# Optimization experiments

Measured on AMD Instinct MI355X. Metric: run time of the kernel, lower is better.

The kernel has to match this reference:

```python
import jax, jax.numpy as jnp
import numpy as np

EPS = 1e-6
NH, DK, DV = 4, 32, 32

def _ln2d(x, w, b):
    # LayerNorm2d: normalize over channel dim (dim=1), biased variance
    mu = jnp.mean(x, axis=1, keepdims=True)
    var = jnp.mean((x - mu) ** 2, axis=1, keepdims=True)
    y = (x - mu) / jnp.sqrt(var + EPS)
    return w[None, :, None, None] * y + b[None, :, None, None]

def _c1x1(w, x):
    # 1x1 conv == per-pixel matmul: w [out,in], x [B,C,H,W]
    return jnp.einsum('oc,bchw->bohw', w, x)

def _shifts(x, r):
    # All (2r+1)^2 zero-padded spatial shifts, row-major (dy,dx) like nn.Unfold.
    B, C, H, W = x.shape
    xp = jnp.pad(x, ((0, 0), (0, 0), (r, r), (r, r)))
    return jnp.stack([xp[:, :, dy:dy + H, dx:dx + W]
                      for dy in range(2 * r + 1) for dx in range(2 * r + 1)], axis=0)

def _local_attn(q, k, v, kernel):
    # Correlation-pyramid local attention: per-pixel q.k over kxk window of k,
    # softmax over window (temperature sqrt(d_k)), weighted sum of v window
    # (weights shared across channels, per ChannelAttention).
    B, _, H, W = q.shape
    r = (kernel - 1) // 2
    K2 = kernel * kernel
    qh = q.reshape(B, NH, DK, H, W)
    ks = _shifts(k, r).reshape(K2, B, NH, DK, H, W)
    corr = jnp.einsum('bncyx,jbncyx->jbnyx', qh, ks)            # [K2,B,NH,H,W]
    attn = jax.nn.softmax(corr / jnp.sqrt(jnp.float32(DK)), axis=0)
    vs = _shifts(v, r).reshape(K2, B, NH, DV, H, W)
    out = jnp.einsum('jbnyx,jbncyx->bncyx', attn, vs)
    return out.reshape(B, NH * DV, H, W)

def _mha(q, k, v, kernel, wq, wk, wv, fc, lnw, lnb):
    resid = q
    heads = _local_attn(_c1x1(wq, q), _c1x1(wk, k), _c1x1(wv, v), kernel)
    out = _c1x1(fc, heads) + resid   # residual BEFORE LN (per source)
    return _ln2d(out, lnw, lnb)

def _ffn(x, w1, b1, w2, b2, lnw, lnb):
    h = jax.nn.relu(_c1x1(w1, x) + b1[None, :, None, None])
    y = _c1x1(w2, h) + b2[None, :, None, None]
    return _ln2d(y, lnw, lnb) + x    # LN BEFORE residual add (per source)

def setup_inputs():
    key = jax.random.key(0)
    ks = jax.random.split(key, 24)
    B, C, H, W = 4, 128, 96, 96
    s = (2.0 / C) ** 0.5
    f = jnp.float32
    return {
        'input1': jax.random.normal(ks[0], (B, C, H, W), f),
        'input2': jax.random.normal(ks[1], (B, C, H, W), f),
        'wq_s': jax.random.normal(ks[2], (NH * DK, C), f) * s,
        'wk_s': jax.random.normal(ks[3], (NH * DK, C), f) * s,
        'wv_s': jax.random.normal(ks[4], (NH * DV, C), f) * s,
        'fc_s': jax.random.normal(ks[5], (C, NH * DV), f) * s,
        'lnw_s': jnp.ones((C,), f),
        'lnb_s': jnp.zeros((C,), f),
        'wq_c': jax.random.normal(ks[6], (NH * DK, C), f) * s,
        'wk_c': jax.random.normal(ks[7], (NH * DK, C), f) * s,
        'wv_c': jax.random.normal(ks[8], (NH * DV, C), f) * s,
        'fc_c': jax.random.normal(ks[9], (C, NH * DV), f) * s,
        'lnw_c': jnp.ones((C,), f),
        'lnb_c': jnp.zeros((C,), f),
        'w1': jax.random.normal(ks[10], (C, C), f) * s,
        'b1': jnp.zeros((C,), f),
        'w2': jax.random.normal(ks[11], (C, C), f) * s,
        'b2': jnp.zeros((C,), f),
        'lnw_f': jnp.ones((C,), f),
        'lnb_f': jnp.zeros((C,), f),
        'kernel': 5,
        'pad': 2,
    }

def reference(input1, input2, wq_s, wk_s, wv_s, fc_s, lnw_s, lnb_s,
              wq_c, wk_c, wv_c, fc_c, lnw_c, lnb_c,
              w1, b1, w2, b2, lnw_f, lnb_f, kernel, pad):
    slf1 = _mha(input1, input1, input1, kernel, wq_s, wk_s, wv_s, fc_s, lnw_s, lnb_s)
    slf2 = _mha(input2, input2, input2, kernel, wq_s, wk_s, wv_s, fc_s, lnw_s, lnb_s)
    crs1 = _mha(slf1, slf2, slf2, kernel, wq_c, wk_c, wv_c, fc_c, lnw_c, lnb_c)
    crs2 = _mha(slf2, slf1, slf1, kernel, wq_c, wk_c, wv_c, fc_c, lnw_c, lnb_c)
    out1 = _ffn(crs1, w1, b1, w2, b2, lnw_f, lnb_f)
    out2 = _ffn(crs2, w1, b1, w2, b2, lnw_f, lnb_f)
    return (out1, out2)
```

## Files before the change

### kernel.cpp

```cpp
#include <hip/hip_runtime.h>
#include <hip/hip_bf16.h>

typedef _Float16 h16;
typedef __attribute__((ext_vector_type(8))) _Float16 f16x8v;
typedef __attribute__((ext_vector_type(2))) _Float16 h2v;
typedef __attribute__((ext_vector_type(4))) float f32x4;
#define DI __device__ __forceinline__

constexpr int CH = 128;
constexpr int HH = 96, WW = 96;
constexpr int HW = HH * WW;
constexpr int NB = 4;
constexpr int NPIX = NB * HW;
constexpr int LDT = 136;
constexpr size_t HP = (size_t)NPIX * 32;
constexpr int GH = NPIX / 64;
constexpr int TY = 4, TX = 32;
constexpr int HYH = TY + 4, HXH = TX + 4;
constexpr int LDC = 40;
constexpr int ATB = NPIX / (TY * TX) * 4;

struct __attribute__((aligned(16))) h16x8 { h16 h[8]; };
struct Set { h16 *q, *k, *v; };

DI float h2f(h16 x) { return (float)x; }
DI h16   f2h(float x) { return (h16)x; }


DI void stage_x_pl(const float* __restrict__ src, h16* xl, int t) {
    #pragma unroll
    for (int i = 0; i < 8; ++i) {
        int id = t + 256 * i, c = id >> 4, p4 = (id & 15) * 4;
        float4 v = *reinterpret_cast<const float4*>(&src[(size_t)c * HW + p4]);
        xl[(p4 + 0) * LDT + c] = f2h(v.x);
        xl[(p4 + 1) * LDT + c] = f2h(v.y);
        xl[(p4 + 2) * LDT + c] = f2h(v.z);
        xl[(p4 + 3) * LDT + c] = f2h(v.w);
    }
}

DI void stage_x_hm(const h16* __restrict__ Tq, h16* xl, int p0, int t) {
    const int px = t >> 2, c8 = (t & 3) * 8;
    #pragma unroll
    for (int h = 0; h < 4; ++h)
        *reinterpret_cast<f16x8v*>(&xl[px * LDT + h * 32 + c8]) =
            *reinterpret_cast<const f16x8v*>(&Tq[(size_t)h * HP + (size_t)(p0 + px) * 32 + c8]);
}

DI void stage_w(const float* __restrict__ w, h16* wl, int t) {
    #pragma unroll
    for (int i = 0; i < 8; ++i) {
        int id = t + 256 * i, o = id >> 4, cc = (id & 15) * 8;
        float4 a = *reinterpret_cast<const float4*>(&w[o * CH + cc]);
        float4 b = *reinterpret_cast<const float4*>(&w[o * CH + cc + 4]);
        h16x8 tmp;
        tmp.h[0] = f2h(a.x); tmp.h[1] = f2h(a.y); tmp.h[2] = f2h(a.z); tmp.h[3] = f2h(a.w);
        tmp.h[4] = f2h(b.x); tmp.h[5] = f2h(b.y); tmp.h[6] = f2h(b.z); tmp.h[7] = f2h(b.w);
        *reinterpret_cast<f16x8v*>(&wl[o * LDT + cc]) = *reinterpret_cast<const f16x8v*>(&tmp);
    }
}

DI void wload(const float* __restrict__ w, f16x8v* pre, int t) {
    #pragma unroll
    for (int i = 0; i < 8; ++i) {
        int id = t + 256 * i, o = id >> 4, cc = (id & 15) * 8;
        float4 a = *reinterpret_cast<const float4*>(&w[o * CH + cc]);
        float4 b = *reinterpret_cast<const float4*>(&w[o * CH + cc + 4]);
        h16x8 tmp;
        tmp.h[0] = f2h(a.x); tmp.h[1] = f2h(a.y); tmp.h[2] = f2h(a.z); tmp.h[3] = f2h(a.w);
        tmp.h[4] = f2h(b.x); tmp.h[5] = f2h(b.y); tmp.h[6] = f2h(b.z); tmp.h[7] = f2h(b.w);
        pre[i] = *reinterpret_cast<const f16x8v*>(&tmp);
    }
}
DI void wcommit(const f16x8v* pre, h16* wl, int t) {
    #pragma unroll
    for (int i = 0; i < 8; ++i) {
        int id = t + 256 * i, o = id >> 4, cc = (id & 15) * 8;
        *reinterpret_cast<f16x8v*>(&wl[o * LDT + cc]) = pre[i];
    }
}

DI void rload(const float* __restrict__ src, float4* rpre, int t) {
    #pragma unroll
    for (int i = 0; i < 8; ++i) {
        int id = t + 256 * i, c = id >> 4, p4 = (id & 15) * 4;
        rpre[i] = *reinterpret_cast<const float4*>(&src[(size_t)c * HW + p4]);
    }
}
DI void rcommit(const float4* rpre, float* rl, int t) {
    #pragma unroll
    for (int i = 0; i < 8; ++i) {
        int id = t + 256 * i, c = id >> 4, p4 = (id & 15) * 4;
        rl[c * 65 + p4 + 0] = rpre[i].x;
        rl[c * 65 + p4 + 1] = rpre[i].y;
        rl[c * 65 + p4 + 2] = rpre[i].z;
        rl[c * 65 + p4 + 3] = rpre[i].w;
    }
}

DI void gemm64(const h16* xl, const h16* wl, int w, int l, f32x4* acc) {
    const int s = l & 15, g = l >> 4;
    #pragma unroll
    for (int ks = 0; ks < 4; ++ks) {
        f16x8v a = *reinterpret_cast<const f16x8v*>(&xl[(16 * w + s) * LDT + ks * 32 + g * 8]);
        #pragma unroll
        for (int n = 0; n < 8; ++n) {
            f16x8v b = *reinterpret_cast<const f16x8v*>(&wl[(16 * n + s) * LDT + ks * 32 + g * 8]);
            acc[n] = __builtin_amdgcn_mfma_f32_16x16x32_f16(a, b, acc[n], 0, 0, 0);
        }
    }
}

DI void qkv_epi(const f32x4* acc, h16* comp, int p0, int w, int l) {
    const int s = l & 15, g = l >> 4;
    #pragma unroll
    for (int n = 0; n < 8; ++n) {
        const int o = 16 * n + s, head = o >> 5, ch = o & 31;
        h16* pl = comp + (size_t)head * HP;
        #pragma unroll
        for (int j = 0; j < 4; ++j) {
            int px = 16 * w + 4 * g + j;
            pl[(size_t)(p0 + px) * 32 + ch] = f2h(acc[n][j]);
        }
    }
}

DI void ln128(float r[8][4], const float* gm, const float* bt, float val[8][4]) {
    #pragma unroll
    for (int j = 0; j < 4; ++j) {
        float sm = 0.f, sq = 0.f;
        #pragma unroll
        for (int n = 0; n < 8; ++n) { float v = r[n][j]; sm += v; sq += v * v; }
        sm += __shfl_xor(sm, 1); sq += __shfl_xor(sq, 1);
        sm += __shfl_xor(sm, 2); sq += __shfl_xor(sq, 2);
        sm += __shfl_xor(sm, 4); sq += __shfl_xor(sq, 4);
        sm += __shfl_xor(sm, 8); sq += __shfl_xor(sq, 8);
        const float mu = sm * (1.f / 128.f);
        const float var = sq * (1.f / 128.f) - mu * mu;
        const float rs = rsqrtf(var + 1e-6f);
        #pragma unroll
        for (int n = 0; n < 8; ++n)
            val[n][j] = gm[n] * (r[n][j] - mu) * rs + bt[n];
    }
}

__global__ __launch_bounds__(256, 2)
void qkv_self_b(const float* __restrict__ x0, const float* __restrict__ x1,
                const float* __restrict__ w0, const float* __restrict__ w1_,
                const float* __restrict__ w2_, Set sA, Set sB) {
    __shared__ h16 xl[64 * LDT];
    __shared__ h16 wl[CH * LDT];
    const int bid = blockIdx.x, half = bid / GH, p0 = (bid % GH) * 64;
    const float* xv = half ? x1 : x0;
    Set S = half ? sB : sA;
    const int t = threadIdx.x;
    const int b = p0 / HW, hw0 = p0 % HW;
    stage_x_pl(xv + (size_t)b * CH * HW + hw0, xl, t);
    stage_w(w0, wl, t);
    __syncthreads();
    const int w = t >> 6, l = t & 63;

    f16x8v pre[8];
    #pragma unroll
    for (int m = 0; m < 3; ++m) {
        h16* comp = (m == 0) ? S.q : ((m == 1) ? S.k : S.v);
        if (m == 0) wload(w1_, pre, t);
        if (m == 1) wload(w2_, pre, t);
        f32x4 acc[8];
        #pragma unroll
        for (int n = 0; n < 8; ++n) acc[n] = {0.f, 0.f, 0.f, 0.f};
        gemm64(xl, wl, w, l, acc);
        qkv_epi(acc, comp, p0, w, l);
        if (m < 2) {
            __syncthreads();
            wcommit(pre, wl, t);
            __syncthreads();
        }
    }
}

__global__ __launch_bounds__(256)
void attn5b(Set s0, Set s1) {
    __shared__ h16 kv[HYH * HXH * LDC];
    const int bid = blockIdx.x, setId = bid / ATB, id = bid - setId * ATB;
    Set S = setId ? s1 : s0;
    const int n = id & 3, tile = id >> 2;
    const int img = tile / 72, rem = tile % 72, tr = rem / 3, tc = rem % 3;
    const int y0 = tr * TY, x0 = tc * TX;
    const int t = threadIdx.x;
    const int p = t >> 1, half = t & 1, ch16 = half * 16;
    const int ty = p >> 5, tx = p & 31;
    h16* Qh = S.q + (size_t)n * HP;
    const h16* Kh = S.k + (size_t)n * HP;
    const h16* Vh = S.v + (size_t)n * HP;
    const int gp = img * HW + (y0 + ty) * WW + (x0 + tx);
    h16* qp = Qh + (size_t)gp * 32 + ch16;

    f16x8v q0 = *reinterpret_cast<const f16x8v*>(qp);
    f16x8v q1 = *reinterpret_cast<const f16x8v*>(qp + 8);
    {
        const h16 sc = (h16)0.17677669529663689f;
        #pragma unroll
        for (int e = 0; e < 8; ++e) { q0[e] *= sc; q1[e] *= sc; }
    }

    #pragma unroll
    for (int i = 0; i < 5; ++i) {
        int id2 = t + 256 * i;
        if (id2 < 1152) {
            int r = id2 / 144, c = id2 - r * 144, px = c >> 2, c8 = (c & 3) * 8;
            int y = y0 + r - 2, x = x0 + px - 2;
            f16x8v v = {0, 0, 0, 0, 0, 0, 0, 0};
            if ((unsigned)y < (unsigned)HH && (unsigned)x < (unsigned)WW)
                v = *reinterpret_cast<const f16x8v*>(&Kh[((size_t)(img * HW + y * WW + x)) * 32 + c8]);
            *reinterpret_cast<f16x8v*>(&kv[(r * HXH + px) * LDC + c8]) = v;
        }
    }
    __syncthreads();

    float corr[25];
    #pragma unroll
    for (int dy = 0; dy < 5; ++dy)
        #pragma unroll
        for (int dx = 0; dx < 5; ++dx) {
            const h16* kp = &kv[((ty + dy) * HXH + tx + dx) * LDC + ch16];
            f16x8v k0 = *reinterpret_cast<const f16x8v*>(kp);
            f16x8v k1 = *reinterpret_cast<const f16x8v*>(kp + 8);
            float s;
#if __has_builtin(__builtin_amdgcn_fdot2)
            s = __builtin_amdgcn_fdot2(h2v{q0[0], q0[1]}, h2v{k0[0], k0[1]}, 0.f, false);
            s = __builtin_amdgcn_fdot2(h2v{q0[2], q0[3]}, h2v{k0[2], k0[3]}, s, false);
            s = __builtin_amdgcn_fdot2(h2v{q0[4], q0[5]}, h2v{k0[4], k0[5]}, s, false);
            s = __builtin_amdgcn_fdot2(h2v{q0[6], q0[7]}, h2v{k0[6], k0[7]}, s, false);
            s = __builtin_amdgcn_fdot2(h2v{q1[0], q1[1]}, h2v{k1[0], k1[1]}, s, false);
            s = __builtin_amdgcn_fdot2(h2v{q1[2], q1[3]}, h2v{k1[2], k1[3]}, s, false);
            s = __builtin_amdgcn_fdot2(h2v{q1[4], q1[5]}, h2v{k1[4], k1[5]}, s, false);
            s = __builtin_amdgcn_fdot2(h2v{q1[6], q1[7]}, h2v{k1[6], k1[7]}, s, false);
#else
            s = 0.f;
            #pragma unroll
            for (int e = 0; e < 8; ++e) s += h2f(q0[e]) * h2f(k0[e]);
            #pragma unroll
            for (int e = 0; e < 8; ++e) s += h2f(q1[e]) * h2f(k1[e]);
#endif
            s += __shfl_xor(s, 1);
            corr[dy * 5 + dx] = s;
        }

    float m = corr[0];
    #pragma unroll
    for (int j = 1; j < 25; ++j) m = fmaxf(m, corr[j]);
    float sum = 0.f;
    #pragma unroll
    for (int j = 0; j < 25; ++j) {
        float e = __expf(corr[j] - m);
        corr[j] = e; sum += e;
    }
    const float inv = 1.f / sum;

    __syncthreads();
    #pragma unroll
    for (int i = 0; i < 5; ++i) {
        int id2 = t + 256 * i;
        if (id2 < 1152) {
            int r = id2 / 144, c = id2 - r * 144, px = c >> 2, c8 = (c & 3) * 8;
            int y = y0 + r - 2, x = x0 + px - 2;
            f16x8v v = {0, 0, 0, 0, 0, 0, 0, 0};
            if ((unsigned)y < (unsigned)HH && (unsigned)x < (unsigned)WW)
                v = *reinterpret_cast<const f16x8v*>(&Vh[((size_t)(img * HW + y * WW + x)) * 32 + c8]);
            *reinterpret_cast<f16x8v*>(&kv[(r * HXH + px) * LDC + c8]) = v;
        }
    }
    __syncthreads();

    f16x8v o0 = {0, 0, 0, 0, 0, 0, 0, 0};
    f16x8v o1 = {0, 0, 0, 0, 0, 0, 0, 0};
    #pragma unroll
    for (int dy = 0; dy < 5; ++dy)
        #pragma unroll
        for (int dx = 0; dx < 5; ++dx) {
            const h16 ah = f2h(corr[dy * 5 + dx]);
            const f16x8v av = {ah, ah, ah, ah, ah, ah, ah, ah};
            const h16* vp = &kv[((ty + dy) * HXH + tx + dx) * LDC + ch16];
            f16x8v v0 = *reinterpret_cast<const f16x8v*>(vp);
            f16x8v v1 = *reinterpret_cast<const f16x8v*>(vp + 8);
            o0 += av * v0;
            o1 += av * v1;
        }
    {
        const h16 ih = f2h(inv);
        const f16x8v iv = {ih, ih, ih, ih, ih, ih, ih, ih};
        o0 *= iv; o1 *= iv;
    }
    *reinterpret_cast<f16x8v*>(qp)     = o0;
    *reinterpret_cast<f16x8v*>(qp + 8) = o1;
}

__global__ __launch_bounds__(256, 2)
void fcx1_b(const h16* __restrict__ tA, const h16* __restrict__ tB,
            const float* __restrict__ in1, const float* __restrict__ in2,
            const float* __restrict__ wfc, const float* __restrict__ gamma,
            const float* __restrict__ beta,
            const float* __restrict__ wq, const float* __restrict__ wk,
            const float* __restrict__ wv,
            h16* __restrict__ x1g, h16* __restrict__ x2g, Set c1, Set c2) {
    __shared__ h16 xl[64 * LDT];
    __shared__ __align__(16) char wsm[CH * LDT * 2];
    h16*   wl = (h16*)wsm;
    float* rl = (float*)wsm;
    const int bid = blockIdx.x, half = bid / GH, p0 = (bid % GH) * 64;
    const h16*   tin = half ? tB : tA;
    const float* inr = half ? in2 : in1;
    h16*         xg  = half ? x2g : x1g;
    Set own   = half ? c2 : c1;
    Set other = half ? c1 : c2;
    const int t = threadIdx.x;
    const int w = t >> 6, l = t & 63, s = l & 15, g4 = l >> 4;
    const int b = p0 / HW, hw0 = p0 % HW;

    stage_x_hm(tin, xl, p0, t);
    stage_w(wfc, wl, t);
    float4 rpre[8];
    rload(inr + (size_t)b * CH * HW + hw0, rpre, t);
    __syncthreads();

    f32x4 accF[8];
    #pragma unroll
    for (int n = 0; n < 8; ++n) accF[n] = {0.f, 0.f, 0.f, 0.f};
    gemm64(xl, wl, w, l, accF);
    __syncthreads();

    rcommit(rpre, rl, t);
    f16x8v pre[8];
    wload(wq, pre, t);
    __syncthreads();

    h16 vX[8][4];
    {
        float gm[8], bt[8], r[8][4], val[8][4];
        #pragma unroll
        for (int n = 0; n < 8; ++n) { gm[n] = gamma[16 * n + s]; bt[n] = beta[16 * n + s]; }
        #pragma unroll
        for (int n = 0; n < 8; ++n) {
            const int o = 16 * n + s;
            #pragma unroll
            for (int j = 0; j < 4; ++j) {
                const int px = 16 * w + 4 * g4 + j;
                r[n][j] = accF[n][j] + rl[o * 65 + px];
            }
        }
        ln128(r, gm, bt, val);
        #pragma unroll
        for (int n = 0; n < 8; ++n)
            #pragma unroll
            for (int j = 0; j < 4; ++j) vX[n][j] = f2h(val[n][j]);
    }
    __syncthreads();
    #pragma unroll
    for (int n = 0; n < 8; ++n) {
        const int o = 16 * n + s;
        #pragma unroll
        for (int j = 0; j < 4; ++j) {
            const int px = 16 * w + 4 * g4 + j;
            xl[px * LDT + o] = vX[n][j];
            xg[(size_t)(p0 + px) * CH + o] = vX[n][j];
        }
    }
    wcommit(pre, wl, t);
    __syncthreads();
    {
        f32x4 acc[8];
        #pragma unroll
        for (int n = 0; n < 8; ++n) acc[n] = {0.f, 0.f, 0.f, 0.f};
        wload(wk, pre, t);
        gemm64(xl, wl, w, l, acc);
        qkv_epi(acc, own.q, p0, w, l);
    }
    __syncthreads();
    wcommit(pre, wl, t);
    __syncthreads();
    {
        f32x4 acc[8];
        #pragma unroll
        for (int n = 0; n < 8; ++n) acc[n] = {0.f, 0.f, 0.f, 0.f};
        wload(wv, pre, t);
        gemm64(xl, wl, w, l, acc);
        qkv_epi(acc, other.k, p0, w, l);
    }
    __syncthreads();
    wcommit(pre, wl, t);
    __syncthreads();
    {
        f32x4 acc[8];
        #pragma unroll
        for (int n = 0; n < 8; ++n) acc[n] = {0.f, 0.f, 0.f, 0.f};
        gemm64(xl, wl, w, l, acc);
        qkv_epi(acc, other.v, p0, w, l);
    }
}

__global__ __launch_bounds__(256, 2)
void ffn_ln_b(const h16* __restrict__ t0, const h16* __restrict__ t1,
              const h16* __restrict__ x0, const h16* __restrict__ x1,
              const float* __restrict__ wfc, const float* __restrict__ gc,
              const float* __restrict__ bc,
              const float* __restrict__ w1m, const float* __restrict__ b1v,
              const float* __restrict__ w2m, const float* __restrict__ b2v,
              const float* __restrict__ gf, const float* __restrict__ bf,
              float* __restrict__ o0, float* __restrict__ o1) {
    __shared__ __align__(16) char smem[64 * LDT * 2 * 2 + CH * LDT * 2];
    h16*   xl = (h16*)smem;
    h16*   yl = (h16*)(smem + 64 * LDT * 2);
    h16*   wl = (h16*)(smem + 64 * LDT * 2 * 2);
    float* ll = (float*)(smem + 64 * LDT * 2 * 2);
    const int bid = blockIdx.x, half = bid / GH, p0 = (bid % GH) * 64;
    const h16* tin = half ? t1 : t0;
    const h16* xg  = half ? x1 : x0;
    float* outp = half ? o1 : o0;
    const int t = threadIdx.x;
    const int w = t >> 6, l = t & 63, s = l & 15, g4 = l >> 4;

    stage_x_hm(tin, xl, p0, t);
    stage_w(wfc, wl, t);
    __syncthreads();

    h16 yv[8][4];
    {
        f32x4 acc[8];
        #pragma unroll
        for (int n = 0; n < 8; ++n) acc[n] = {0.f, 0.f, 0.f, 0.f};
        gemm64(xl, wl, w, l, acc);
        float gm[8], bt[8], r[8][4], val[8][4];
        #pragma unroll
        for (int n = 0; n < 8; ++n) { gm[n] = gc[16 * n + s]; bt[n] = bc[16 * n + s]; }
        #pragma unroll
        for (int n = 0; n < 8; ++n) {
            const int o = 16 * n + s;
            #pragma unroll
            for (int j = 0; j < 4; ++j) {
                const int px = 16 * w + 4 * g4 + j;
                r[n][j] = acc[n][j] + h2f(xg[(size_t)(p0 + px) * CH + o]);
            }
        }
        ln128(r, gm, bt, val);
        #pragma unroll
        for (int n = 0; n < 8; ++n)
            #pragma unroll
            for (int j = 0; j < 4; ++j) yv[n][j] = f2h(val[n][j]);
    }
    __syncthreads();
    #pragma unroll
    for (int n = 0; n < 8; ++n) {
        const int o = 16 * n + s;
        #pragma unroll
        for (int j = 0; j < 4; ++j)
            yl[(16 * w + 4 * g4 + j) * LDT + o] = yv[n][j];
    }
    stage_w(w1m, wl, t);
    __syncthreads();

    {
        f32x4 acc[8];
        #pragma unroll
        for (int n = 0; n < 8; ++n) acc[n] = {0.f, 0.f, 0.f, 0.f};
        gemm64(yl, wl, w, l, acc);
        #pragma unroll
        for (int n = 0; n < 8; ++n) {
            const int o = 16 * n + s;
            const float bv = b1v[o];
            #pragma unroll
            for (int j = 0; j < 4; ++j)
                xl[(16 * w + 4 * g4 + j) * LDT + o] = f2h(fmaxf(acc[n][j] + bv, 0.f));
        }
    }
    __syncthreads();
    stage_w(w2m, wl, t);
    __syncthreads();

    float val[8][4];
    {
        f32x4 acc[8];
        #pragma unroll
        for (int n = 0; n < 8; ++n) acc[n] = {0.f, 0.f, 0.f, 0.f};
        gemm64(xl, wl, w, l, acc);
        float gm[8], bt[8], r[8][4];
        #pragma unroll
        for (int n = 0; n < 8; ++n) { gm[n] = gf[16 * n + s]; bt[n] = bf[16 * n + s]; }
        #pragma unroll
        for (int n = 0; n < 8; ++n) {
            const int o = 16 * n + s;
            const float bv = b2v[o];
            #pragma unroll
            for (int j = 0; j < 4; ++j) r[n][j] = acc[n][j] + bv;
        }
        ln128(r, gm, bt, val);
        #pragma unroll
        for (int n = 0; n < 8; ++n) {
            const int o = 16 * n + s;
            #pragma unroll
            for (int j = 0; j < 4; ++j)
                val[n][j] += h2f(yl[(16 * w + 4 * g4 + j) * LDT + o]);
        }
    }
    __syncthreads();
    #pragma unroll
    for (int n = 0; n < 8; ++n) {
        const int o = 16 * n + s;
        #pragma unroll
        for (int j = 0; j < 4; ++j) ll[o * 65 + 16 * w + 4 * g4 + j] = val[n][j];
    }
    __syncthreads();
    const int b = p0 / HW, hw0 = p0 % HW;
    #pragma unroll
    for (int i = 0; i < 8; ++i) {
        int id = t + 256 * i, c = id >> 4, p4 = (id & 15) * 4;
        float4 v = { ll[c * 65 + p4], ll[c * 65 + p4 + 1],
                     ll[c * 65 + p4 + 2], ll[c * 65 + p4 + 3] };
        *reinterpret_cast<float4*>(&outp[(size_t)b * CH * HW + (size_t)c * HW + hw0 + p4]) = v;
    }
}

extern "C" void kernel_launch(void* const* d_in, const int* in_sizes, int n_in,
                              void* d_out, int out_size, void* d_ws, size_t ws_size,
                              hipStream_t stream) {
    (void)in_sizes; (void)n_in; (void)out_size; (void)ws_size;
    const float* in1  = (const float*)d_in[0];
    const float* in2  = (const float*)d_in[1];
    const float* wq_s = (const float*)d_in[2];
    const float* wk_s = (const float*)d_in[3];
    const float* wv_s = (const float*)d_in[4];
    const float* fc_s = (const float*)d_in[5];
    const float* lnw_s= (const float*)d_in[6];
    const float* lnb_s= (const float*)d_in[7];
    const float* wq_c = (const float*)d_in[8];
    const float* wk_c = (const float*)d_in[9];
    const float* wv_c = (const float*)d_in[10];
    const float* fc_c = (const float*)d_in[11];
    const float* lnw_c= (const float*)d_in[12];
    const float* lnb_c= (const float*)d_in[13];
    const float* w1   = (const float*)d_in[14];
    const float* b1   = (const float*)d_in[15];
    const float* w2   = (const float*)d_in[16];
    const float* b2   = (const float*)d_in[17];
    const float* lnw_f= (const float*)d_in[18];
    const float* lnb_f= (const float*)d_in[19];

    const size_t BUF  = (size_t)NPIX * CH;
    const size_t BUFB = BUF * 2;
    char* ws = (char*)d_ws;
    h16* W0 = (h16*)(ws + 0 * BUFB);
    h16* W1 = (h16*)(ws + 1 * BUFB);
    h16* W2 = (h16*)(ws + 2 * BUFB);
    h16* W3 = (h16*)(ws + 3 * BUFB);
    h16* D0 = (h16*)d_out;
    h16* D1 = (h16*)((char*)d_out + 1 * BUFB);
    h16* D2 = (h16*)((char*)d_out + 2 * BUFB);
    h16* D3 = (h16*)((char*)d_out + 3 * BUFB);
    float* out1 = (float*)d_out;
    float* out2 = (float*)d_out + BUF;

    const dim3 B(256);

    Set SA = {W0, D0, D1};
    Set SB = {W1, D2, D3};
    h16* X1 = W2;
    h16* X2 = W3;
    Set C1 = {W0, D0, D1};
    Set C2 = {W1, D2, D3};

    qkv_self_b<<<dim3(2 * GH), B, 0, stream>>>(in1, in2, wq_s, wk_s, wv_s, SA, SB);
    attn5b<<<dim3(2 * ATB), B, 0, stream>>>(SA, SB);
    fcx1_b<<<dim3(2 * GH), B, 0, stream>>>(SA.q, SB.q, in1, in2,
                                           fc_s, lnw_s, lnb_s,
                                           wq_c, wk_c, wv_c, X1, X2, C1, C2);
    attn5b<<<dim3(2 * ATB), B, 0, stream>>>(C1, C2);
    ffn_ln_b<<<dim3(2 * GH), B, 0, stream>>>(C1.q, C2.q, X1, X2,
                                             fc_c, lnw_c, lnb_c,
                                             w1, b1, w2, b2, lnw_f, lnb_f,
                                             out1, out2);
}
```

Before: 152.7 us.

## Split fc+LN kernel from cross QKV projection into separate wider-grid kernel

The fused fc+residual+LN+QKV kernel is split in two. The first kernel computes the fc projection, residual and LayerNorm and writes X with coalesced vector stores. A second kernel launches three times as many blocks, one per projection (q, k, v) per pixel tile, so the three GEMMs run in parallel instead of sequentially within a block. The cost is an extra launch, a global round trip of X, and reloading X once per projection.

```diff
diff --git a/kernel.cpp b/kernel.cpp
--- a/kernel.cpp
+++ b/kernel.cpp
@@ -26,6 +26,15 @@
 DI float h2f(h16 x) { return (float)x; }
 DI h16   f2h(float x) { return (h16)x; }
 
+
+DI void stage_x_cl(const h16* __restrict__ src, int ldx, h16* xl, int t) {
+    #pragma unroll
+    for (int i = 0; i < 4; ++i) {
+        int id = t + 256 * i, px = id >> 4, cc = (id & 15) * 8;
+        *reinterpret_cast<f16x8v*>(&xl[px * LDT + cc]) =
+            *reinterpret_cast<const f16x8v*>(&src[(size_t)px * ldx + cc]);
+    }
+}
 
 DI void stage_x_pl(const float* __restrict__ src, h16* xl, int t) {
     #pragma unroll
@@ -297,13 +306,11 @@
 }
 
 __global__ __launch_bounds__(256, 2)
-void fcx1_b(const h16* __restrict__ tA, const h16* __restrict__ tB,
-            const float* __restrict__ in1, const float* __restrict__ in2,
-            const float* __restrict__ wfc, const float* __restrict__ gamma,
-            const float* __restrict__ beta,
-            const float* __restrict__ wq, const float* __restrict__ wk,
-            const float* __restrict__ wv,
-            h16* __restrict__ x1g, h16* __restrict__ x2g, Set c1, Set c2) {
+void fcx_a(const h16* __restrict__ tA, const h16* __restrict__ tB,
+           const float* __restrict__ in1, const float* __restrict__ in2,
+           const float* __restrict__ wfc, const float* __restrict__ gamma,
+           const float* __restrict__ beta,
+           h16* __restrict__ x1g, h16* __restrict__ x2g) {
     __shared__ h16 xl[64 * LDT];
     __shared__ __align__(16) char wsm[CH * LDT * 2];
     h16*   wl = (h16*)wsm;
@@ -312,8 +319,6 @@
     const h16*   tin = half ? tB : tA;
     const float* inr = half ? in2 : in1;
     h16*         xg  = half ? x2g : x1g;
-    Set own   = half ? c2 : c1;
-    Set other = half ? c1 : c2;
     const int t = threadIdx.x;
     const int w = t >> 6, l = t & 63, s = l & 15, g4 = l >> 4;
     const int b = p0 / HW, hw0 = p0 % HW;
@@ -331,72 +336,61 @@
     __syncthreads();
 
     rcommit(rpre, rl, t);
-    f16x8v pre[8];
-    wload(wq, pre, t);
-    __syncthreads();
-
-    h16 vX[8][4];
-    {
-        float gm[8], bt[8], r[8][4], val[8][4];
-        #pragma unroll
-        for (int n = 0; n < 8; ++n) { gm[n] = gamma[16 * n + s]; bt[n] = beta[16 * n + s]; }
-        #pragma unroll
-        for (int n = 0; n < 8; ++n) {
-            const int o = 16 * n + s;
-            #pragma unroll
-            for (int j = 0; j < 4; ++j) {
-                const int px = 16 * w + 4 * g4 + j;
-                r[n][j] = accF[n][j] + rl[o * 65 + px];
-            }
-        }
-        ln128(r, gm, bt, val);
-        #pragma unroll
-        for (int n = 0; n < 8; ++n)
-            #pragma unroll
-            for (int j = 0; j < 4; ++j) vX[n][j] = f2h(val[n][j]);
-    }
-    __syncthreads();
+    __syncthreads();
+
+    float gm[8], bt[8], r[8][4], val[8][4];
+    #pragma unroll
+    for (int n = 0; n < 8; ++n) { gm[n] = gamma[16 * n + s]; bt[n] = beta[16 * n + s]; }
     #pragma unroll
     for (int n = 0; n < 8; ++n) {
         const int o = 16 * n + s;
         #pragma unroll
-        for (int j = 0; j < 4; ++j) {
-            const int px = 16 * w + 4 * g4 + j;
-            xl[px * LDT + o] = vX[n][j];
-            xg[(size_t)(p0 + px) * CH + o] = vX[n][j];
-        }
-    }
-    wcommit(pre, wl, t);
-    __syncthreads();
-    {
-        f32x4 acc[8];
-        #pragma unroll
-        for (int n = 0; n < 8; ++n) acc[n] = {0.f, 0.f, 0.f, 0.f};
-        wload(wk, pre, t);
-        gemm64(xl, wl, w, l, acc);
-        qkv_epi(acc, own.q, p0, w, l);
-    }
-    __syncthreads();
-    wcommit(pre, wl, t);
-    __syncthreads();
-    {
-        f32x4 acc[8];
-        #pragma unroll
-        for (int n = 0; n < 8; ++n) acc[n] = {0.f, 0.f, 0.f, 0.f};
-        wload(wv, pre, t);
-        gemm64(xl, wl, w, l, acc);
-        qkv_epi(acc, other.k, p0, w, l);
-    }
-    __syncthreads();
-    wcommit(pre, wl, t);
-    __syncthreads();
-    {
-        f32x4 acc[8];
-        #pragma unroll
-        for (int n = 0; n < 8; ++n) acc[n] = {0.f, 0.f, 0.f, 0.f};
-        gemm64(xl, wl, w, l, acc);
-        qkv_epi(acc, other.v, p0, w, l);
-    }
+        for (int j = 0; j < 4; ++j)
+            r[n][j] = accF[n][j] + rl[o * 65 + (16 * w + 4 * g4 + j)];
+    }
+    ln128(r, gm, bt, val);
+    #pragma unroll
+    for (int n = 0; n < 8; ++n) {
+        const int o = 16 * n + s;
+        #pragma unroll
+        for (int j = 0; j < 4; ++j)
+            xl[(16 * w + 4 * g4 + j) * LDT + o] = f2h(val[n][j]);
+    }
+    __syncthreads();
+    #pragma unroll
+    for (int i = 0; i < 4; ++i) {
+        int id = t + 256 * i, px = id >> 4, c8 = (id & 15) * 8;
+        *reinterpret_cast<f16x8v*>(&xg[(size_t)(p0 + px) * CH + c8]) =
+            *reinterpret_cast<const f16x8v*>(&xl[px * LDT + c8]);
+    }
+}
+
+__global__ __launch_bounds__(256, 2)
+void fcx_b2(const h16* __restrict__ x1, const h16* __restrict__ x2,
+            const float* __restrict__ wq, const float* __restrict__ wk,
+            const float* __restrict__ wv, Set c1, Set c2) {
+    __shared__ h16 xl[64 * LDT];
+    __shared__ h16 wl[CH * LDT];
+    const int bid = blockIdx.x;
+    const int mvar = bid / (2 * GH);
+    const int rem  = bid - mvar * 2 * GH;
+    const int half = rem / GH, p0 = (rem % GH) * 64;
+    const h16* xs = half ? x2 : x1;
+    Set own   = half ? c2 : c1;
+    Set other = half ? c1 : c2;
+    h16* comp = (mvar == 0) ? own.q : ((mvar == 1) ? other.k : other.v);
+    const float* wm = (mvar == 0) ? wq : ((mvar == 1) ? wk : wv);
+    const int t = threadIdx.x, w = t >> 6, l = t & 63;
+
+    stage_x_cl(xs + (size_t)p0 * CH, CH, xl, t);
+    stage_w(wm, wl, t);
+    __syncthreads();
+
+    f32x4 acc[8];
+    #pragma unroll
+    for (int n = 0; n < 8; ++n) acc[n] = {0.f, 0.f, 0.f, 0.f};
+    gemm64(xl, wl, w, l, acc);
+    qkv_epi(acc, comp, p0, w, l);
 }
 
 __global__ __launch_bounds__(256, 2)
@@ -570,9 +564,9 @@
 
     qkv_self_b<<<dim3(2 * GH), B, 0, stream>>>(in1, in2, wq_s, wk_s, wv_s, SA, SB);
     attn5b<<<dim3(2 * ATB), B, 0, stream>>>(SA, SB);
-    fcx1_b<<<dim3(2 * GH), B, 0, stream>>>(SA.q, SB.q, in1, in2,
-                                           fc_s, lnw_s, lnb_s,
-                                           wq_c, wk_c, wv_c, X1, X2, C1, C2);
+    fcx_a<<<dim3(2 * GH), B, 0, stream>>>(SA.q, SB.q, in1, in2,
+                                          fc_s, lnw_s, lnb_s, X1, X2);
+    fcx_b2<<<dim3(6 * GH), B, 0, stream>>>(X1, X2, wq_c, wk_c, wv_c, C1, C2);
     attn5b<<<dim3(2 * ATB), B, 0, stream>>>(C1, C2);
     ffn_ln_b<<<dim3(2 * GH), B, 0, stream>>>(C1.q, C2.q, X1, X2,
                                              fc_c, lnw_c, lnb_c,
```

New measurement: 156.2 us. 1.02x slower.
